# Performance work log

Hardware: AMD Instinct MI355X
Metric: run time of the kernel (lower is better)

## Reference

```python
import jax, jax.numpy as jnp
import numpy as np

ALPHA, BETA, TAU = 0.3, 1.0, 0.07
TOP_K, TOP_KC = 16, 16
CLASS_W = jnp.array([2.5, 2.0, 1.0, 5.0, 4.0, 5.0, 5.0], dtype=jnp.float32)

def _conf_mat():
    m = np.ones((7, 7), dtype=np.float32)
    pairs = {(0, 1): 3.0, (1, 0): 3.0, (0, 2): 2.0, (2, 0): 2.0, (1, 2): 2.0,
             (2, 1): 2.0, (5, 0): 2.0, (0, 5): 2.0, (4, 6): 2.0, (6, 4): 2.0}
    for (i, j), w in pairs.items():
        m[i, j] = w
    return jnp.asarray(m)
CONF_MAT = _conf_mat()

def _l2norm(x, eps=1e-12):
    return x / jnp.maximum(jnp.linalg.norm(x, axis=-1, keepdims=True), eps)

def setup_inputs() -> dict:
    key = jax.random.key(0)
    ks = jax.random.split(key, 9)
    B, P, C, D, K = 512, 196, 80, 512, 16
    return {
        'disease_logits': jax.random.normal(ks[0], (B, 7), jnp.float32),
        'concept_scores': jax.random.normal(ks[1], (B, C), jnp.float32),
        'labels': jax.random.randint(ks[2], (B,), 0, 7),
        'patch_similarity': jax.random.normal(ks[3], (B, P, C), jnp.float32),
        'patch_features': jax.random.normal(ks[4], (B, P, D), jnp.float32),
        'cav_vectors': jax.random.normal(ks[5], (C, D), jnp.float32),
        'w_vote': jax.random.uniform(ks[6], (7, C), jnp.float32),
        'text_embeddings': jax.random.normal(ks[7], (C, D), jnp.float32),
        'top_k_indices': jax.random.randint(ks[8], (B, K), 0, C),
    }

def reference(disease_logits, concept_scores, labels, patch_similarity,
              patch_features, cav_vectors, w_vote, text_embeddings, top_k_indices):
    B = disease_logits.shape[0]
    # ---- focal loss (classification) ----
    logp = jax.nn.log_softmax(disease_logits, axis=1)
    ce = -jnp.take_along_axis(logp, labels[:, None], axis=1)[:, 0]
    pt = jnp.exp(-ce)
    focal_w = (1.0 - pt) ** 2.5
    sample_w = CLASS_W[labels]
    pred = jnp.argmax(disease_logits, axis=1)
    conf_w = CONF_MAT[labels, pred]
    max_prob = jnp.exp(jnp.max(logp, axis=1))
    conf_pen = 1.0 + (max_prob < 0.7).astype(jnp.float32) * 0.5
    loss_cls = jnp.mean(0.25 * focal_w * ce * sample_w * conf_w * conf_pen)

    # ---- cross-view alignment loss ----
    patch_norm = _l2norm(patch_features)                          # [B,P,D]
    cav_norm = cav_vectors / (jnp.linalg.norm(cav_vectors, axis=-1, keepdims=True) + 1e-8)
    w_vote_norm = _l2norm(w_vote)                                  # [7,C]
    # top patches per concept: topk over patch axis
    ps_t = jnp.swapaxes(patch_similarity, 1, 2)                    # [B,C,P]
    _, top_pidx = jax.lax.top_k(ps_t, TOP_K)                       # [B,C,K]
    _, top_cidx = jax.lax.top_k(concept_scores, TOP_KC)            # [B,Kc]
    b_ar = jnp.arange(B)
    tpi = top_pidx[b_ar[:, None], top_cidx]                        # [B,Kc,K]
    gathered = patch_norm[b_ar[:, None, None], tpi]                # [B,Kc,K,D]
    mean_patch = gathered.mean(axis=2)                             # [B,Kc,D]
    cav_sel = cav_norm[top_cidx]                                   # [B,Kc,D]
    num = jnp.einsum('bkd,bkd->bk', mean_patch, cav_sel)
    den = jnp.linalg.norm(mean_patch, axis=-1) * jnp.linalg.norm(cav_sel, axis=-1)
    sim = num / jnp.maximum(den, 1e-8)                             # [B,Kc]
    pos_mask = w_vote_norm > 0.1                                   # [7,C]
    is_pos = pos_mask[labels[:, None], top_cidx]                   # [B,Kc]
    pos_count = jnp.maximum(jnp.sum(is_pos), 1).astype(jnp.float32)
    neg_count = jnp.maximum(jnp.sum(~is_pos), 1).astype(jnp.float32)
    dw = w_vote_norm[labels[:, None], top_cidx]                    # [B,Kc]
    loss_align = jnp.sum(jnp.where(is_pos,
                                   dw * (1.0 - sim) / pos_count,
                                   0.1 * (1.0 + sim) / neg_count))

    # ---- text anchor loss (top_k_indices path, clamped InfoNCE) ----
    text_norm = _l2norm(text_embeddings)                           # [C,D]
    cav_b = cav_norm[top_k_indices]                                # [B,K,D]
    text_b = text_norm[top_k_indices]                              # [B,K,D]
    sim_t = jnp.einsum('bid,bjd->bij', cav_b, text_b) / TAU
    sim_t = jnp.clip(sim_t, -100.0, 100.0)
    lse = jax.nn.logsumexp(sim_t, axis=-1)                         # [B,K]
    diag = jnp.diagonal(sim_t, axis1=1, axis2=2)                   # [B,K]
    loss_text = jnp.mean(lse - diag)

    total = loss_cls + ALPHA * loss_align + BETA * loss_text
    return total
```

## Files before the change

### kernel.cpp

```cpp
#include <hip/hip_runtime.h>
#include <math.h>

#define P 196
#define C 80
#define D 512
#define CH 128

#define WS_CLS   0
#define AP_BASE  1024
#define TP_BASE  40960

__device__ __constant__ float d_class_w[7] = {2.5f, 2.0f, 1.0f, 5.0f, 4.0f, 5.0f, 5.0f};
__device__ __constant__ float d_conf[49] = {
    1,3,2,1,1,2,1,
    3,1,2,1,1,1,1,
    2,2,1,1,1,1,1,
    1,1,1,1,1,1,1,
    1,1,1,1,1,1,2,
    2,1,1,1,1,1,1,
    1,1,1,1,2,1,1};

__device__ __forceinline__ float wave_sum(float v) {
  #pragma unroll
  for (int off = 32; off; off >>= 1) v += __shfl_xor(v, off, 64);
  return v;
}

__device__ __forceinline__ float dot4(float4 a, float4 b) {
  return a.x*b.x + a.y*b.y + a.z*b.z + a.w*b.w;
}

__device__ __forceinline__ unsigned mono(float v) {
  unsigned u = __float_as_uint(v);
  return u ^ (((unsigned)((int)u >> 31)) | 0x80000000u);
}

#define PIDX(j) ((int)((((j) < 8) ? (pk0 >> (8 * (j))) : (pk1 >> (8 * ((j) - 8)))) & 0xFFull))
#define ROWP(j) (pfb + (size_t)PIDX(j) * (D / 4))

__launch_bounds__(256)
__global__ void k_fat(const float* __restrict__ cs, const int* __restrict__ labels,
                      const float* __restrict__ ps, const float* __restrict__ pf,
                      const float* __restrict__ cav, const float* __restrict__ wv,
                      const float* __restrict__ text, const int* __restrict__ tki,
                      const float* __restrict__ logits,
                      float* __restrict__ f, int B, int swz) {
  __shared__ float stx[16][CH + 4];
  __shared__ int sidx[16];
  __shared__ float rowsum[16];
  __shared__ float part[4];

  int bid = blockIdx.x;
  int tid = threadIdx.x, lane = tid & 63, wave = tid >> 6;

  if (bid < 4 * B) {
    int b, g;
    if (swz) {
      int xcd = bid & 7, rest = bid >> 3;
      g = rest & 3;
      b = (rest >> 2) * 8 + xcd;
    } else {
      b = bid >> 2; g = bid & 3;
    }
    int rank = g * 4 + wave;
    int l = labels[b];

    int c;
    {
      float v0 = cs[(size_t)b * C + lane];
      float v1 = (lane < C - 64) ? cs[(size_t)b * C + 64 + lane] : -INFINITY;
      unsigned u0 = mono(v0), u1 = mono(v1);
      unsigned prefix = 0u;
      #pragma unroll
      for (int bit = 31; bit >= 0; --bit) {
        unsigned cand = prefix | (1u << bit);
        int cnt = __popcll(__ballot(u0 >= cand)) + __popcll(__ballot(u1 >= cand));
        if (cnt >= 16) prefix = cand;
      }
      unsigned long long g0 = __ballot(u0 > prefix);
      unsigned long long g1 = __ballot(u1 > prefix);
      unsigned long long e0 = __ballot(u0 == prefix);
      unsigned long long e1 = __ballot(u1 == prefix);
      int take = 16 - __popcll(g0) - __popcll(g1);
      while (take > 0 && e0) { g0 |= e0 & (~e0 + 1ull); e0 &= e0 - 1ull; take--; }
      while (take > 0 && e1) { g1 |= e1 & (~e1 + 1ull); e1 &= e1 - 1ull; take--; }
      int p0 = __popcll(g0);
      if (rank < p0) {
        unsigned long long m = g0;
        int r = rank; while (r--) m &= m - 1ull;
        c = __ffsll(m) - 1;
      } else {
        unsigned long long m = g1;
        int r = rank - p0; while (r--) m &= m - 1ull;
        c = 64 + __ffsll(m) - 1;
      }
    }

    unsigned long long pk0 = 0ull, pk1 = 0ull;
    {
      const float* col = ps + (size_t)b * P * C + c;
      float v0 = col[(size_t)lane * C];
      float v1 = col[(size_t)(64 + lane) * C];
      float v2 = col[(size_t)(128 + lane) * C];
      float v3 = (lane < P - 192) ? col[(size_t)(192 + lane) * C] : -INFINITY;
      unsigned u0 = mono(v0), u1 = mono(v1), u2 = mono(v2), u3 = mono(v3);
      unsigned prefix = 0u;
      #pragma unroll
      for (int bit = 31; bit >= 0; --bit) {
        unsigned cand = prefix | (1u << bit);
        int cnt = __popcll(__ballot(u0 >= cand)) + __popcll(__ballot(u1 >= cand))
                + __popcll(__ballot(u2 >= cand)) + __popcll(__ballot(u3 >= cand));
        if (cnt >= 16) prefix = cand;
      }
      unsigned long long s0 = __ballot(u0 > prefix);
      unsigned long long s1 = __ballot(u1 > prefix);
      unsigned long long s2 = __ballot(u2 > prefix);
      unsigned long long s3 = __ballot(u3 > prefix);
      unsigned long long e0 = __ballot(u0 == prefix);
      unsigned long long e1 = __ballot(u1 == prefix);
      unsigned long long e2 = __ballot(u2 == prefix);
      unsigned long long e3 = __ballot(u3 == prefix);
      int take = 16 - __popcll(s0) - __popcll(s1) - __popcll(s2) - __popcll(s3);
      while (take > 0 && e0) { s0 |= e0 & (~e0 + 1ull); e0 &= e0 - 1ull; take--; }
      while (take > 0 && e1) { s1 |= e1 & (~e1 + 1ull); e1 &= e1 - 1ull; take--; }
      while (take > 0 && e2) { s2 |= e2 & (~e2 + 1ull); e2 &= e2 - 1ull; take--; }
      while (take > 0 && e3) { s3 |= e3 & (~e3 + 1ull); e3 &= e3 - 1ull; take--; }
      int cnt = 0;
      unsigned long long m;
      m = s0; while (m) { unsigned long long p = (unsigned long long)(__ffsll(m) - 1);
        if (cnt < 8) pk0 |= p << (8 * cnt); else pk1 |= p << (8 * (cnt - 8));
        cnt++; m &= m - 1ull; }
      m = s1; while (m) { unsigned long long p = (unsigned long long)(63 + __ffsll(m));
        if (cnt < 8) pk0 |= p << (8 * cnt); else pk1 |= p << (8 * (cnt - 8));
        cnt++; m &= m - 1ull; }
      m = s2; while (m) { unsigned long long p = (unsigned long long)(127 + __ffsll(m));
        if (cnt < 8) pk0 |= p << (8 * cnt); else pk1 |= p << (8 * (cnt - 8));
        cnt++; m &= m - 1ull; }
      m = s3; while (m) { unsigned long long p = (unsigned long long)(191 + __ffsll(m));
        if (cnt < 8) pk0 |= p << (8 * cnt); else pk1 |= p << (8 * (cnt - 8));
        cnt++; m &= m - 1ull; }
    }

    float4 a0 = make_float4(0, 0, 0, 0), a1 = make_float4(0, 0, 0, 0);
    {
      const float4* pfb = (const float4*)(pf + (size_t)b * P * D);
      float4 A0 = ROWP(0)[lane], A1 = ROWP(0)[64 + lane];
      float4 B0 = ROWP(1)[lane], B1 = ROWP(1)[64 + lane];
      #pragma unroll
      for (int j = 0; j < 16; j += 2) {
        float4 N0, N1, M0, M1;
        if (j < 14) {
          const float4* rn = ROWP(j + 2);
          const float4* rm = ROWP(j + 3);
          N0 = rn[lane]; N1 = rn[64 + lane];
          M0 = rm[lane]; M1 = rm[64 + lane];
        }
        float ssA = dot4(A0, A0) + dot4(A1, A1);
        float ssB = dot4(B0, B0) + dot4(B1, B1);
        #pragma unroll
        for (int off = 32; off; off >>= 1) {
          ssA += __shfl_xor(ssA, off, 64);
          ssB += __shfl_xor(ssB, off, 64);
        }
        float scA = 1.f / fmaxf(sqrtf(ssA), 1e-12f);
        float scB = 1.f / fmaxf(sqrtf(ssB), 1e-12f);
        a0.x += scA * A0.x + scB * B0.x; a0.y += scA * A0.y + scB * B0.y;
        a0.z += scA * A0.z + scB * B0.z; a0.w += scA * A0.w + scB * B0.w;
        a1.x += scA * A1.x + scB * B1.x; a1.y += scA * A1.y + scB * B1.y;
        a1.z += scA * A1.z + scB * B1.z; a1.w += scA * A1.w + scB * B1.w;
        if (j < 14) { A0 = N0; A1 = N1; B0 = M0; B1 = M1; }
      }
    }
    const float inv16 = 1.f / 16.f;
    a0.x *= inv16; a0.y *= inv16; a0.z *= inv16; a0.w *= inv16;
    a1.x *= inv16; a1.y *= inv16; a1.z *= inv16; a1.w *= inv16;

    {
      const float4* crow = (const float4*)(cav + (size_t)c * D);
      float4 c0 = crow[lane], c1 = crow[64 + lane];
      float nr2 = dot4(c0, c0) + dot4(c1, c1);
      float numr = dot4(a0, c0) + dot4(a1, c1);
      float nm = dot4(a0, a0) + dot4(a1, a1);
      float wx = wv[l * C + lane];
      float wy = (lane < C - 64) ? wv[l * C + 64 + lane] : 0.f;
      float wn2 = wx * wx + wy * wy;
      #pragma unroll
      for (int off = 1; off < 64; off <<= 1) {
        nr2 += __shfl_xor(nr2, off, 64);
        numr += __shfl_xor(numr, off, 64);
        nm += __shfl_xor(nm, off, 64);
        wn2 += __shfl_xor(wn2, off, 64);
      }
      if (lane == 0) {
        float n = sqrtf(nr2);
        float csc = 1.f / (n + 1e-8f);
        float num = numr * csc;
        float ncn = n * csc;
        float sim = num / fmaxf(sqrtf(nm) * ncn, 1e-8f);
        float wvs = 1.f / fmaxf(sqrtf(wn2), 1e-12f);
        float dw = wv[l * C + c] * wvs;
        float sp = 0.f, sn = 0.f, cp = 0.f;
        if (dw > 0.1f) { sp = dw * (1.f - sim); cp = 1.f; }
        else           { sn = 1.f + sim; }
        float* prt = f + AP_BASE + (size_t)(b * 16 + rank) * 4;
        prt[0] = sp; prt[1] = sn; prt[2] = cp;
      }
    }
    return;
  }

  if (bid < 5 * B) {
    int b = bid - 4 * B;
    if (tid < 16) sidx[tid] = tki[b * 16 + tid];
    __syncthreads();
    int i = tid >> 4, j = tid & 15;
    const float* cr = cav + (size_t)sidx[i] * D;
    float dotp = 0.f, ssc = 0.f, sst = 0.f;
    for (int ch = 0; ch < D; ch += CH) {
      for (int t = tid; t < 16 * CH; t += 256) {
        int r = t >> 7, d = t & (CH - 1);
        stx[r][d] = text[(size_t)sidx[r] * D + ch + d];
      }
      __syncthreads();
      const float4* cr4 = (const float4*)(cr + ch);
      #pragma unroll 8
      for (int d = 0; d < CH; d += 4) {
        float4 a = cr4[d >> 2];
        float4 t4 = *(const float4*)&stx[j][d];
        dotp += dot4(a, t4);
        ssc += dot4(a, a);
        sst += dot4(t4, t4);
      }
      __syncthreads();
    }
    float cscale = 1.f / (sqrtf(ssc) + 1e-8f);
    float tscale = 1.f / fmaxf(sqrtf(sst), 1e-12f);
    float s = dotp * cscale * tscale * (1.f / 0.07f);
    s = fminf(fmaxf(s, -100.f), 100.f);
    float m = s;
    #pragma unroll
    for (int off = 1; off < 16; off <<= 1) m = fmaxf(m, __shfl_xor(m, off, 64));
    float e = expf(s - m);
    #pragma unroll
    for (int off = 1; off < 16; off <<= 1) e += __shfl_xor(e, off, 64);
    float lse = m + logf(e);
    float sd = __shfl(s, ((i & 3) << 4) | i, 64);
    if (j == 0) rowsum[i] = lse - sd;
    __syncthreads();
    if (tid == 0) {
      float acc = 0.f;
      #pragma unroll
      for (int r = 0; r < 16; r++) acc += rowsum[r];
      f[TP_BASE + b] = acc;
    }
    return;
  }

  {
    float val = 0.f;
    for (int i = tid; i < B; i += 256) {
      float x[7];
      #pragma unroll
      for (int c = 0; c < 7; c++) x[c] = logits[i * 7 + c];
      int pred = 0; float m = x[0];
      #pragma unroll
      for (int c = 1; c < 7; c++) if (x[c] > m) { m = x[c]; pred = c; }
      float s = 0.f;
      #pragma unroll
      for (int c = 0; c < 7; c++) s += expf(x[c] - m);
      float lse = m + logf(s);
      int l = labels[i];
      float logp_l = x[l] - lse;
      float ce = -logp_l;
      float pt = expf(logp_l);
      float focal = powf(1.f - pt, 2.5f);
      float maxp = expf(m - lse);
      float pen = (maxp < 0.7f) ? 1.5f : 1.f;
      val += 0.25f * focal * ce * d_class_w[l] * d_conf[l * 7 + pred] * pen;
    }
    val = wave_sum(val);
    if (lane == 0) part[wave] = val;
    __syncthreads();
    if (tid == 0) f[WS_CLS] = part[0] + part[1] + part[2] + part[3];
  }
}

__launch_bounds__(256)
__global__ void k_final(const float* __restrict__ f, float* __restrict__ out, int B) {
  __shared__ float red[4][4];
  int tid = threadIdx.x, lane = tid & 63, wave = tid >> 6;
  float sp = 0.f, sn = 0.f, cp = 0.f, tx = 0.f;
  const float4* ap4 = (const float4*)(f + AP_BASE);
  for (int t = tid; t < B * 16; t += 256) {
    float4 p = ap4[t];
    sp += p.x; sn += p.y; cp += p.z;
  }
  for (int b = tid; b < B; b += 256) tx += f[TP_BASE + b];
  sp = wave_sum(sp); sn = wave_sum(sn); cp = wave_sum(cp); tx = wave_sum(tx);
  if (lane == 0) {
    red[wave][0] = sp; red[wave][1] = sn; red[wave][2] = cp; red[wave][3] = tx;
  }
  __syncthreads();
  if (tid == 0) {
    float SP = 0.f, SN = 0.f, CP = 0.f, TX = 0.f;
    #pragma unroll
    for (int w = 0; w < 4; w++) {
      SP += red[w][0]; SN += red[w][1]; CP += red[w][2]; TX += red[w][3];
    }
    float total_pairs = (float)B * 16.f;
    float pc = fmaxf(CP, 1.f);
    float ncnt = fmaxf(total_pairs - CP, 1.f);
    float align = SP / pc + 0.1f * SN / ncnt;
    out[0] = f[WS_CLS] / (float)B + 0.3f * align + TX / total_pairs;
  }
}

extern "C" void kernel_launch(void* const* d_in, const int* in_sizes, int n_in,
                              void* d_out, int out_size, void* d_ws, size_t ws_size,
                              hipStream_t stream) {
  const float* dl     = (const float*)d_in[0];
  const float* cs     = (const float*)d_in[1];
  const int*   labels = (const int*)d_in[2];
  const float* ps     = (const float*)d_in[3];
  const float* pf     = (const float*)d_in[4];
  const float* cav    = (const float*)d_in[5];
  const float* wv     = (const float*)d_in[6];
  const float* text   = (const float*)d_in[7];
  const int*   tki    = (const int*)d_in[8];
  float* out = (float*)d_out;
  float* f   = (float*)d_ws;
  int B = in_sizes[0] / 7;
  int swz = (B % 8 == 0) ? 1 : 0;

  hipLaunchKernelGGL(k_fat, dim3(5 * B + 1), dim3(256), 0, stream,
                     cs, labels, ps, pf, cav, wv, text, tki, dl, f, B, swz);
  hipLaunchKernelGGL(k_final, dim3(1), dim3(256), 0, stream, f, out, B);
}
```

Before: 73.58 us.

## Reorder text blocks first, batch patch-norm loads, and vectorize text staging

Moves the text-anchor InfoNCE blocks to the front of the grid so they get scheduled first, and vectorizes their shared-memory staging of text rows with float4 loads. In the alignment blocks, all 16 selected patch rows are loaded up front and their squared norms reduced together in one batched shuffle tree. The rows are then re-read for the weighted accumulation, and the cav and w_vote loads are hoisted early. This aims for more memory-level parallelism and fewer serialized reductions, at the cost of more registers and a second read of each patch row (likely an L2 hit).

```diff
diff --git a/kernel.cpp b/kernel.cpp
--- a/kernel.cpp
+++ b/kernel.cpp
@@ -53,17 +53,71 @@
   int bid = blockIdx.x;
   int tid = threadIdx.x, lane = tid & 63, wave = tid >> 6;
 
-  if (bid < 4 * B) {
+  if (bid < B) {
+    int b = bid;
+    if (tid < 16) sidx[tid] = tki[b * 16 + tid];
+    __syncthreads();
+    int i = tid >> 4, j = tid & 15;
+    const float* cr = cav + (size_t)sidx[i] * D;
+    float dotp = 0.f, ssc = 0.f, sst = 0.f;
+    for (int ch = 0; ch < D; ch += CH) {
+      #pragma unroll
+      for (int t = tid; t < 16 * (CH / 4); t += 256) {
+        int r = t >> 5, d4 = t & 31;
+        float4 v = *(const float4*)(text + (size_t)sidx[r] * D + ch + d4 * 4);
+        *(float4*)&stx[r][d4 * 4] = v;
+      }
+      __syncthreads();
+      const float4* cr4 = (const float4*)(cr + ch);
+      #pragma unroll 8
+      for (int d = 0; d < CH; d += 4) {
+        float4 a = cr4[d >> 2];
+        float4 t4 = *(const float4*)&stx[j][d];
+        dotp += dot4(a, t4);
+        ssc += dot4(a, a);
+        sst += dot4(t4, t4);
+      }
+      __syncthreads();
+    }
+    float cscale = 1.f / (sqrtf(ssc) + 1e-8f);
+    float tscale = 1.f / fmaxf(sqrtf(sst), 1e-12f);
+    float s = dotp * cscale * tscale * (1.f / 0.07f);
+    s = fminf(fmaxf(s, -100.f), 100.f);
+    float m = s;
+    #pragma unroll
+    for (int off = 1; off < 16; off <<= 1) m = fmaxf(m, __shfl_xor(m, off, 64));
+    float e = expf(s - m);
+    #pragma unroll
+    for (int off = 1; off < 16; off <<= 1) e += __shfl_xor(e, off, 64);
+    float lse = m + logf(e);
+    float sd = __shfl(s, ((i & 3) << 4) | i, 64);
+    if (j == 0) rowsum[i] = lse - sd;
+    __syncthreads();
+    if (tid == 0) {
+      float acc = 0.f;
+      #pragma unroll
+      for (int r = 0; r < 16; r++) acc += rowsum[r];
+      f[TP_BASE + b] = acc;
+    }
+    return;
+  }
+
+  if (bid < 5 * B) {
+    int mb = bid - B;
     int b, g;
     if (swz) {
-      int xcd = bid & 7, rest = bid >> 3;
+      int xcd = mb & 7, rest = mb >> 3;
       g = rest & 3;
       b = (rest >> 2) * 8 + xcd;
     } else {
-      b = bid >> 2; g = bid & 3;
+      b = mb >> 2; g = mb & 3;
     }
     int rank = g * 4 + wave;
     int l = labels[b];
+
+    float wx = wv[l * C + lane];
+    float wy = (lane < C - 64) ? wv[l * C + 64 + lane] : 0.f;
+    float wn2 = wx * wx + wy * wy;
 
     int c;
     {
@@ -141,55 +195,55 @@
         cnt++; m &= m - 1ull; }
     }
 
+    const float4* crow = (const float4*)(cav + (size_t)c * D);
+    float4 c0 = crow[lane], c1 = crow[64 + lane];
+    float nr2 = dot4(c0, c0) + dot4(c1, c1);
+
+    const float4* pfb = (const float4*)(pf + (size_t)b * P * D);
+    float ssl[16];
+    #pragma unroll
+    for (int j = 0; j < 8; j++) {
+      const float4* row = ROWP(j);
+      float4 r0 = row[lane], r1 = row[64 + lane];
+      ssl[j] = dot4(r0, r0) + dot4(r1, r1);
+    }
+    #pragma unroll
+    for (int j = 8; j < 16; j++) {
+      const float4* row = ROWP(j);
+      float4 r0 = row[lane], r1 = row[64 + lane];
+      ssl[j] = dot4(r0, r0) + dot4(r1, r1);
+    }
+
+    #pragma unroll
+    for (int off = 32; off; off >>= 1) {
+      #pragma unroll
+      for (int j = 0; j < 16; j++) ssl[j] += __shfl_xor(ssl[j], off, 64);
+      nr2 += __shfl_xor(nr2, off, 64);
+      wn2 += __shfl_xor(wn2, off, 64);
+    }
+    #pragma unroll
+    for (int j = 0; j < 16; j++) ssl[j] = 1.f / fmaxf(sqrtf(ssl[j]), 1e-12f);
+
     float4 a0 = make_float4(0, 0, 0, 0), a1 = make_float4(0, 0, 0, 0);
-    {
-      const float4* pfb = (const float4*)(pf + (size_t)b * P * D);
-      float4 A0 = ROWP(0)[lane], A1 = ROWP(0)[64 + lane];
-      float4 B0 = ROWP(1)[lane], B1 = ROWP(1)[64 + lane];
-      #pragma unroll
-      for (int j = 0; j < 16; j += 2) {
-        float4 N0, N1, M0, M1;
-        if (j < 14) {
-          const float4* rn = ROWP(j + 2);
-          const float4* rm = ROWP(j + 3);
-          N0 = rn[lane]; N1 = rn[64 + lane];
-          M0 = rm[lane]; M1 = rm[64 + lane];
-        }
-        float ssA = dot4(A0, A0) + dot4(A1, A1);
-        float ssB = dot4(B0, B0) + dot4(B1, B1);
-        #pragma unroll
-        for (int off = 32; off; off >>= 1) {
-          ssA += __shfl_xor(ssA, off, 64);
-          ssB += __shfl_xor(ssB, off, 64);
-        }
-        float scA = 1.f / fmaxf(sqrtf(ssA), 1e-12f);
-        float scB = 1.f / fmaxf(sqrtf(ssB), 1e-12f);
-        a0.x += scA * A0.x + scB * B0.x; a0.y += scA * A0.y + scB * B0.y;
-        a0.z += scA * A0.z + scB * B0.z; a0.w += scA * A0.w + scB * B0.w;
-        a1.x += scA * A1.x + scB * B1.x; a1.y += scA * A1.y + scB * B1.y;
-        a1.z += scA * A1.z + scB * B1.z; a1.w += scA * A1.w + scB * B1.w;
-        if (j < 14) { A0 = N0; A1 = N1; B0 = M0; B1 = M1; }
-      }
+    #pragma unroll
+    for (int j = 0; j < 16; j++) {
+      const float4* row = ROWP(j);
+      float4 r0 = row[lane], r1 = row[64 + lane];
+      float sc = ssl[j];
+      a0.x += sc * r0.x; a0.y += sc * r0.y; a0.z += sc * r0.z; a0.w += sc * r0.w;
+      a1.x += sc * r1.x; a1.y += sc * r1.y; a1.z += sc * r1.z; a1.w += sc * r1.w;
     }
     const float inv16 = 1.f / 16.f;
     a0.x *= inv16; a0.y *= inv16; a0.z *= inv16; a0.w *= inv16;
     a1.x *= inv16; a1.y *= inv16; a1.z *= inv16; a1.w *= inv16;
 
     {
-      const float4* crow = (const float4*)(cav + (size_t)c * D);
-      float4 c0 = crow[lane], c1 = crow[64 + lane];
-      float nr2 = dot4(c0, c0) + dot4(c1, c1);
       float numr = dot4(a0, c0) + dot4(a1, c1);
       float nm = dot4(a0, a0) + dot4(a1, a1);
-      float wx = wv[l * C + lane];
-      float wy = (lane < C - 64) ? wv[l * C + 64 + lane] : 0.f;
-      float wn2 = wx * wx + wy * wy;
       #pragma unroll
       for (int off = 1; off < 64; off <<= 1) {
-        nr2 += __shfl_xor(nr2, off, 64);
         numr += __shfl_xor(numr, off, 64);
         nm += __shfl_xor(nm, off, 64);
-        wn2 += __shfl_xor(wn2, off, 64);
       }
       if (lane == 0) {
         float n = sqrtf(nr2);
@@ -205,53 +259,6 @@
         float* prt = f + AP_BASE + (size_t)(b * 16 + rank) * 4;
         prt[0] = sp; prt[1] = sn; prt[2] = cp;
       }
-    }
-    return;
-  }
-
-  if (bid < 5 * B) {
-    int b = bid - 4 * B;
-    if (tid < 16) sidx[tid] = tki[b * 16 + tid];
-    __syncthreads();
-    int i = tid >> 4, j = tid & 15;
-    const float* cr = cav + (size_t)sidx[i] * D;
-    float dotp = 0.f, ssc = 0.f, sst = 0.f;
-    for (int ch = 0; ch < D; ch += CH) {
-      for (int t = tid; t < 16 * CH; t += 256) {
-        int r = t >> 7, d = t & (CH - 1);
-        stx[r][d] = text[(size_t)sidx[r] * D + ch + d];
-      }
-      __syncthreads();
-      const float4* cr4 = (const float4*)(cr + ch);
-      #pragma unroll 8
-      for (int d = 0; d < CH; d += 4) {
-        float4 a = cr4[d >> 2];
-        float4 t4 = *(const float4*)&stx[j][d];
-        dotp += dot4(a, t4);
-        ssc += dot4(a, a);
-        sst += dot4(t4, t4);
-      }
-      __syncthreads();
-    }
-    float cscale = 1.f / (sqrtf(ssc) + 1e-8f);
-    float tscale = 1.f / fmaxf(sqrtf(sst), 1e-12f);
-    float s = dotp * cscale * tscale * (1.f / 0.07f);
-    s = fminf(fmaxf(s, -100.f), 100.f);
-    float m = s;
-    #pragma unroll
-    for (int off = 1; off < 16; off <<= 1) m = fmaxf(m, __shfl_xor(m, off, 64));
-    float e = expf(s - m);
-    #pragma unroll
-    for (int off = 1; off < 16; off <<= 1) e += __shfl_xor(e, off, 64);
-    float lse = m + logf(e);
-    float sd = __shfl(s, ((i & 3) << 4) | i, 64);
-    if (j == 0) rowsum[i] = lse - sd;
-    __syncthreads();
-    if (tid == 0) {
-      float acc = 0.f;
-      #pragma unroll
-      for (int r = 0; r < 16; r++) acc += rowsum[r];
-      f[TP_BASE + b] = acc;
     }
     return;
   }
```

Result: faster. 59.55 us, median of 2 (-19.1%).
